# Optimization experiments

Hardware: AMD Instinct MI355X
Metric: run time of the kernel (lower is better)

Reference implementation:

```python
import jax, jax.numpy as jnp
import numpy as np
import math

N, C, T, V = 8, 256, 128, 25
H, HC = 8, 32            # num_heads, head_channels
W, DIL = 3, 1            # window, dilation
O = 256                  # out_channels
PAD = (W + (W - 1) * (DIL - 1) - 1) // 2
B, L = N * T, W * V


def _ln(x, g, b):
    m = jnp.mean(x, -1, keepdims=True)
    v = jnp.var(x, -1, keepdims=True)
    return (x - m) * jax.lax.rsqrt(v + 1e-5) * g + b


def setup_inputs() -> dict:
    key = jax.random.key(0)
    ks = iter(jax.random.split(key, 40))
    def w(shape):
        return jax.random.normal(next(ks), shape, jnp.float32) * 0.02
    d = {"x": jax.random.normal(next(ks), (N, C, T, V), jnp.float32)}
    d.update(
        ln1_g=jnp.ones((C,)), ln1_b=jnp.zeros((C,)),
        Wq=w((C, C)), bq=jnp.zeros((C,)), Wqa=w((C, H)), bqa=jnp.zeros((H,)),
        Wk=w((C, C)), bk=jnp.zeros((C,)), Wka=w((C, H)), bka=jnp.zeros((H,)),
        Wv=w((C, C)), bv=jnp.zeros((C,)), Wt=w((C, C)), bt=jnp.zeros((C,)),
        Wp=w((C, C)), bp=jnp.zeros((C,)),
        ffn_g=jnp.ones((C,)), ffn_b=jnp.zeros((C,)),
        W1=w((C, C)), b1=jnp.zeros((C,)), W2=w((C, C)), b2=jnp.zeros((C,)),
        tn_g=jnp.ones((C,)), tn_b=jnp.zeros((C,)),
        c1_w=w((C, O)), c1_b=jnp.zeros((O,)),
        c2_w=w((W, O, O)), c2_b=jnp.zeros((O,)),
    )
    return d


def reference(x, ln1_g, ln1_b, Wq, bq, Wqa, bqa, Wk, bk, Wka, bka, Wv, bv,
              Wt, bt, Wp, bp, ffn_g, ffn_b, W1, b1, W2, b2, tn_g, tn_b,
              c1_w, c1_b, c2_w, c2_b):
    scale = 1.0 / math.sqrt(HC)
    # ---- Unfold over time: build window of frames around each t (nn.Unfold) ----
    xp = jnp.pad(x, ((0, 0), (0, 0), (PAD, PAD), (0, 0)))
    win = jnp.stack([jax.lax.dynamic_slice_in_dim(xp, k * DIL, T, 2) for k in range(W)], 2)  # (N,C,W,T,V)
    seq = win.transpose(0, 3, 2, 4, 1).reshape(B, L, C)  # (N*T, W*V, C)

    sep = lambda z: z.reshape(B, L, H, HC).transpose(0, 2, 1, 3)  # (B,H,L,HC)
    grp = lambda z: z.transpose(0, 2, 1, 3).reshape(B, -1, C)

    # ---- SpatioTemporalAttention (eval: dropouts off) ----
    nx = _ln(seq, ln1_g, ln1_b)
    q = nx @ Wq + bq                                            # (B,L,C)
    qw = jax.nn.softmax((q @ Wqa + bqa).transpose(0, 2, 1) * scale, axis=-1)  # (B,H,L)
    pq = jnp.einsum('bhl,bhlc->bhc', qw, sep(q)).reshape(B, 1, C)             # pooled query
    keys = nx @ Wk + bk
    kw = jax.nn.softmax(((keys * pq) @ Wka + bka).transpose(0, 2, 1) * scale, axis=-1)
    pk = jnp.einsum('bhl,bhlc->bhc', kw, sep(keys))             # pooled key (B,H,HC)
    vals = sep(nx @ Wv + bv)
    kv = grp(vals * pk[:, :, None, :]) @ Wt + bt                # (B,L,C)
    attn = (kv + q) @ Wp + bp                                   # residual-in-heads == plain add

    # ---- AttentionBranch residual + FFN ----
    att = attn + seq
    f = _ln(att, ffn_g, ffn_b)
    y = jax.nn.gelu(f @ W1 + b1, approximate=False) @ W2 + b2 + att  # (B,L,C)

    # ---- temporal branch: LN -> regroup frames -> 1x1 conv -> GELU -> (W,1) conv stride W ----
    t5 = _ln(y, tn_g, tn_b).reshape(N, T, W, V, C)
    h = jax.nn.gelu(t5 @ c1_w + c1_b, approximate=False)        # (N,T,W,V,O)
    out = jnp.einsum('ntwvi,wio->ntvo', h, c2_w) + c2_b         # stride==kernel conv == window contraction
    return out.transpose(0, 3, 1, 2)                            # (N,O,T,V)
```

## Files before the change

kernel.cpp:

```cpp
#include <hip/hip_runtime.h>


#define DI __device__ __forceinline__

constexpr int CC   = 256;
constexpr int CL   = 75;
constexpr int CV   = 25;
constexpr int CT   = 128;
constexpr int TP   = 130;
constexpr int MPAD = 8 * TP * CV;
constexpr int MBL  = 1024 * CL;
constexpr int MOUT = 8 * CT * CV;
constexpr float SM_SCALE = 0.17677669529663687f;

typedef __bf16 bf16x8 __attribute__((ext_vector_type(8)));
typedef float f32x4 __attribute__((ext_vector_type(4)));

DI float bf2f(unsigned short u) { return __uint_as_float(((unsigned)u) << 16); }
DI float bf2f_lo(unsigned u) { return __uint_as_float(u << 16); }
DI float bf2f_hi(unsigned u) { return __uint_as_float(u & 0xffff0000u); }
DI unsigned short f2bf(float f) {
  unsigned u = __float_as_uint(f);
  u += 0x7fffu + ((u >> 16) & 1u);
  return (unsigned short)(u >> 16);
}
DI unsigned packbf(float a, float b) {
  return (unsigned)f2bf(a) | ((unsigned)f2bf(b) << 16);
}
DI float geluf(float x) { return 0.5f * x * (1.f + erff(x * 0.70710678118654752440f)); }

DI void gll16(const unsigned short* g, unsigned short* l) {
  __builtin_amdgcn_global_load_lds(
      (const __attribute__((address_space(1))) unsigned int*)g,
      (__attribute__((address_space(3))) unsigned int*)l, 16, 0, 0);
}

DI int arow(int r) {
  int b = r / CL;
  int l = r - b * CL;
  int w = l / CV;
  int v = l - w * CV;
  int t = b & (CT - 1);
  int n = b >> 7;
  return (n * TP + t + w) * CV + v;
}

__global__ __launch_bounds__(256) void k_transpose(const float* __restrict__ x,
                                                   unsigned short* __restrict__ xtp) {
  __shared__ float tile[32][33];
  const int n = blockIdx.z;
  const int c0 = blockIdx.x * 32;
  const int tv0 = blockIdx.y * 32;
  const int tx = threadIdx.x & 31, ty = threadIdx.x >> 5;
#pragma unroll
  for (int j = 0; j < 32; j += 8) {
    tile[ty + j][tx] = x[((size_t)(n * CC + c0 + ty + j)) * 3200 + tv0 + tx];
  }
  __syncthreads();
#pragma unroll
  for (int j = 0; j < 32; j += 8) {
    int tv = tv0 + ty + j;
    int st = tv / CV, v = tv - st * CV;
    size_t row = ((size_t)n * TP + st + 1) * CV + v;
    xtp[row * CC + c0 + tx] = f2bf(tile[tx][ty + j]);
  }
}

__global__ __launch_bounds__(256) void k_zero_pad(unsigned short* __restrict__ xtp) {
  int i = blockIdx.x * 256 + threadIdx.x;
  int c = i & 255;
  int rid = i >> 8;
  int n = rid / 50;
  int rem = rid - n * 50;
  int side = rem / 25;
  int v = rem - side * 25;
  size_t row = ((size_t)n * TP + side * (TP - 1)) * CV + v;
  xtp[row * CC + c] = 0;
}

struct TJobs {
  const float* src[10];
  unsigned short* dst[10];
// ... 20 lines not shown
__global__ __launch_bounds__(256) void k_wtwp(const float* __restrict__ Wt,
                                              const float* __restrict__ Wp,
                                              unsigned short* __restrict__ fused) {
  __shared__ float wrow[256];
  const int k = blockIdx.x, n = threadIdx.x;
  wrow[n] = Wt[(size_t)k * 256 + n];
  __syncthreads();
  float acc = 0.f;
  for (int j = 0; j < 256; ++j) acc = fmaf(wrow[j], Wp[(size_t)j * 256 + n], acc);
  fused[(size_t)n * 512 + k] = f2bf(acc);
}

__global__ __launch_bounds__(256) void k_bias2(const float* __restrict__ bt,
                                               const float* __restrict__ Wp,
                                               const float* __restrict__ bp,
                                               const float* __restrict__ bq,
                                               const float* __restrict__ bk,
                                               const float* __restrict__ bv,
                                               float* __restrict__ bias2,
                                               float* __restrict__ bias3) {
  const int n = threadIdx.x;
  float acc = bp[n];
  for (int j = 0; j < 256; ++j) acc = fmaf(bt[j], Wp[(size_t)j * 256 + n], acc);
  bias2[n] = acc;
  bias3[n] = bq[n];
  bias3[256 + n] = bk[n];
  bias3[512 + n] = bv[n];
}

__global__ __launch_bounds__(256) void k_ln4(const unsigned short* __restrict__ X,
                                             const float* __restrict__ g,
                                             const float* __restrict__ b,
                                             unsigned short* __restrict__ Y) {
  const int row = blockIdx.x * 4 + (threadIdx.x >> 6);
  const int lane = threadIdx.x & 63;
  const uint2 u = *(const uint2*)(X + (size_t)row * CC + lane * 4);
  const float x0 = bf2f_lo(u.x), x1 = bf2f_hi(u.x), x2 = bf2f_lo(u.y), x3 = bf2f_hi(u.y);
  float s = x0 + x1 + x2 + x3;
  float q = x0 * x0 + x1 * x1 + x2 * x2 + x3 * x3;
#pragma unroll
  for (int o = 32; o; o >>= 1) { s += __shfl_xor(s, o); q += __shfl_xor(q, o); }
  const float mean = s * (1.f / CC);
  const float var = q * (1.f / CC) - mean * mean;
  const float rs = rsqrtf(var + 1e-5f);
  const float4 g4 = *(const float4*)(g + lane * 4);
  const float4 b4 = *(const float4*)(b + lane * 4);
  uint2 o2;
  o2.x = packbf((x0 - mean) * rs * g4.x + b4.x, (x1 - mean) * rs * g4.y + b4.y);
  o2.y = packbf((x2 - mean) * rs * g4.z + b4.z, (x3 - mean) * rs * g4.w + b4.w);
  *(uint2*)(Y + (size_t)row * CC + lane * 4) = o2;
}

template <int AMODE, int EPI, int KD, bool MULTI>
__global__ __launch_bounds__(512) void k_mgemm(const unsigned short* __restrict__ A,
                                               const unsigned short* __restrict__ BwT,
                                               const float* __restrict__ bias,
                                               unsigned short* __restrict__ Cout,
                                               float* __restrict__ FOut,
                                               int M) {
  if constexpr (MULTI) {
    const int z = blockIdx.y;
    BwT += (size_t)z * (256 * 256);
    bias += z * 256;
    Cout += (size_t)z * MPAD * CC;
  }
  __shared__ unsigned short SH[20480];
  const int tid = threadIdx.x;
  const int lane = tid & 63;
  const int wid = tid >> 6;
  const int wm = wid >> 2, wn = wid & 3;
  const int r0 = blockIdx.x * 64;
  f32x4 acc[2][4] = {};

  const bool sa = tid < 256;
  const int rA = r0 + (tid >> 2);
  const int seg8 = (tid & 3) * 8;
  const bool valid = sa && (rA < M);
  int hrb = 0;
  if (valid && AMODE == 4) {
    const int nb = rA / 3200, rr = rA - nb * 3200;
    const int tq = rr / 25, vq = rr - tq * 25;
    hrb = (nb * CT + tq) * CL + vq;
  }

  auto loadA4 = [&](int k0) -> uint4 {
    uint4 u = make_uint4(0, 0, 0, 0);
    if (!valid) return u;
    const int w = k0 >> 8;
    u = *(const uint4*)(A + (size_t)(hrb + w * CV) * CC + (k0 & 255) + seg8);
    return u;
  };
  auto stageB = [&](int buf, int k0) {
    unsigned short* bs = SH + 4096 + buf * 8192;
#pragma unroll
    for (int pp = 0; pp < 2; ++pp) {
      const int s = tid + pp * 512;
      gll16(BwT + (size_t)(s >> 2) * KD + k0 + (s & 3) * 8, bs + s * 8);
    }
  };
  auto stageAg = [&](int buf, int k0) {
    if (valid) gll16(A + (size_t)rA * CC + k0 + seg8, SH + buf * 2048 + tid * 8);
  };

  stageB(0, 0);
  if constexpr (AMODE == 0) {
    stageAg(0, 0);
  } else {
    const uint4 a0 = loadA4(0);
    if (sa) *(uint4*)(SH + tid * 8) = a0;
  }
  __syncthreads();

  constexpr int NT = KD / 32;
  int cur = 0;
  for (int t = 0; t < NT; ++t) {
    const int nxt = cur ^ 1;
    const bool more = (t + 1 < NT);
    uint4 an;
    if (more) {
      stageB(nxt, (t + 1) * 32);
      if constexpr (AMODE == 0) stageAg(nxt, (t + 1) * 32);
      else an = loadA4((t + 1) * 32);
    }
    const unsigned short* as = SH + cur * 2048;
    const unsigned short* bs = SH + 4096 + cur * 8192;
    bf16x8 af[2], bfr[4];
#pragma unroll
    for (int mi = 0; mi < 2; ++mi)
      af[mi] = *(const bf16x8*)(as + (wm * 32 + mi * 16 + (lane & 15)) * 32 + (lane >> 4) * 8);
#pragma unroll
    for (int ni = 0; ni < 4; ++ni)
      bfr[ni] = *(const bf16x8*)(bs + (wn * 64 + ni * 16 + (lane & 15)) * 32 + (lane >> 4) * 8);
#pragma unroll
    for (int mi = 0; mi < 2; ++mi)
#pragma unroll
      for (int ni = 0; ni < 4; ++ni)
        acc[mi][ni] = __builtin_amdgcn_mfma_f32_16x16x32_bf16(af[mi], bfr[ni], acc[mi][ni], 0, 0, 0);
    if (more) {
      if constexpr (AMODE != 0) {
        if (sa) *(uint4*)(SH + nxt * 2048 + tid * 8) = an;
      }
      __syncthreads();
      cur = nxt;
    }
  }

  const int ln15 = lane & 15, lq = lane >> 4;
  if constexpr (EPI == 4) {
#pragma unroll
    for (int mi = 0; mi < 2; ++mi) {
#pragma unroll
      for (int ni = 0; ni < 4; ++ni) {
        const int col = wn * 64 + ni * 16 + ln15;
        const float bcol = bias[col];
        const int rbase = r0 + wm * 32 + mi * 16 + lq * 4;
        const int nb = rbase / 3200, rr = rbase - nb * 3200;
        float4 v;
        v.x = acc[mi][ni][0] + bcol;
        v.y = acc[mi][ni][1] + bcol;
        v.z = acc[mi][ni][2] + bcol;
        v.w = acc[mi][ni][3] + bcol;
        *(float4*)(FOut + (size_t)nb * 819200 + (size_t)col * 3200 + rr) = v;
      }
    }
  } else {
    constexpr int LDC = 260;
    __syncthreads();
#pragma unroll
    for (int mi = 0; mi < 2; ++mi) {
#pragma unroll
      for (int ni = 0; ni < 4; ++ni) {
        const int col = wn * 64 + ni * 16 + ln15;
        const float bcol = bias[col];
#pragma unroll
        for (int rg = 0; rg < 4; ++rg) {
          const int lrow = wm * 32 + mi * 16 + lq * 4 + rg;
          SH[lrow * LDC + col] = f2bf(acc[mi][ni][rg] + bcol);
        }
      }
    }
    __syncthreads();
#pragma unroll
    for (int i = 0; i < 4; ++i) {
      const int idx = tid + i * 512;
      const int row = idx >> 5, ch = idx & 31;
      const int gr = r0 + row;
      if (gr < M)
        *(uint4*)(Cout + (size_t)gr * CC + ch * 8) = *(const uint4*)&SH[row * LDC + ch * 8];
    }
  }
}

__global__ __launch_bounds__(512) void k_chain(
    const unsigned short* __restrict__ VP, const unsigned short* __restrict__ QP,
    const float* __restrict__ PK, const unsigned short* __restrict__ XTP,
    const unsigned short* __restrict__ fusedB, const float* __restrict__ bias2,
    const unsigned short* __restrict__ W1T, const float* __restrict__ b1,
    const unsigned short* __restrict__ W2T, const float* __restrict__ b2,
    const float* __restrict__ ffn_g, const float* __restrict__ ffn_b,
    const unsigned short* __restrict__ c1wT, const float* __restrict__ c1b,
    const float* __restrict__ tn_g, const float* __restrict__ tn_b,
    unsigned short* __restrict__ Hout) {
  constexpr int LDC = 264;
  __shared__ unsigned short SH[16896 + 4096 + 16384];
  unsigned short* ACT = SH;
  unsigned short* AS = SH + 16896;
  unsigned short* BS = SH + 16896 + 4096;
  const int tid = threadIdx.x;
  const int lane = tid & 63, wid = tid >> 6;
  const int wm = wid >> 2, wn = wid & 3;
  const int ln15 = lane & 15, lq = lane >> 4;
  const int r0 = blockIdx.x * 64;

  const bool sa = tid < 256;
  const int rA = r0 + (tid >> 2);
  const int seg8 = (tid & 3) * 8;
  int ar = 0, bb = 0;
  if (sa) { ar = arow(rA); bb = rA / CL; }

  auto stageB = [&](const unsigned short* BwT, int KD, int buf, int k0) {
    unsigned short* bs = BS + buf * 8192;
#pragma unroll
    for (int pp = 0; pp < 2; ++pp) {
      const int s = tid + pp * 512;
      gll16(BwT + (size_t)(s >> 2) * KD + k0 + (s & 3) * 8, bs + s * 8);
    }
  };
  auto loadA5 = [&](int k0) -> uint4 {
    uint4 u = make_uint4(0, 0, 0, 0);
    if (!sa) return u;
    if (k0 < 256) {
      const int kg = k0 + seg8;
      const uint4 t4 = *(const uint4*)(VP + (size_t)ar * CC + kg);
      const float* sv = PK + bb * CC + kg;
      const float4 s0 = *(const float4*)sv;
      const float4 s1 = *(const float4*)(sv + 4);
      u.x = packbf(bf2f_lo(t4.x) * s0.x, bf2f_hi(t4.x) * s0.y);
      u.y = packbf(bf2f_lo(t4.y) * s0.z, bf2f_hi(t4.y) * s0.w);
      u.z = packbf(bf2f_lo(t4.z) * s1.x, bf2f_hi(t4.z) * s1.y);
      u.w = packbf(bf2f_lo(t4.w) * s1.z, bf2f_hi(t4.w) * s1.w);
    } else {
      u = *(const uint4*)(QP + (size_t)ar * CC + (k0 - 256) + seg8);
    }
    return u;
  };
  auto ln_inplace = [&](const float* g, const float* b) {
    const float4 g4 = *(const float4*)(g + lane * 4);
    const float4 b4 = *(const float4*)(b + lane * 4);
#pragma unroll
    for (int rr = 0; rr < 8; ++rr) {
      const int row = wid * 8 + rr;
      const uint2 u = *(const uint2*)(ACT + row * LDC + lane * 4);
      const float x0 = bf2f_lo(u.x), x1 = bf2f_hi(u.x);
      const float x2 = bf2f_lo(u.y), x3 = bf2f_hi(u.y);
      float s = x0 + x1 + x2 + x3;
      float q = x0 * x0 + x1 * x1 + x2 * x2 + x3 * x3;
#pragma unroll
      for (int o = 32; o; o >>= 1) { s += __shfl_xor(s, o); q += __shfl_xor(q, o); }
      const float mean = s * (1.f / CC);
      const float var = q * (1.f / CC) - mean * mean;
      const float rs = rsqrtf(var + 1e-5f);
      uint2 o2;
      o2.x = packbf((x0 - mean) * rs * g4.x + b4.x, (x1 - mean) * rs * g4.y + b4.y);
      o2.y = packbf((x2 - mean) * rs * g4.z + b4.z, (x3 - mean) * rs * g4.w + b4.w);
      *(uint2*)(ACT + row * LDC + lane * 4) = o2;
    }
  };
  auto gemmACT = [&](const unsigned short* BwT, f32x4 (&a)[2][4]) {
    int c2 = 0;
    for (int t = 0; t < 8; ++t) {
      if (t + 1 < 8) stageB(BwT, 256, c2 ^ 1, (t + 1) * 32);
      bf16x8 af[2], bfr[4];
#pragma unroll
      for (int mi = 0; mi < 2; ++mi)
        af[mi] = *(const bf16x8*)(ACT + (wm * 32 + mi * 16 + ln15) * LDC + t * 32 + lq * 8);
#pragma unroll
      for (int ni = 0; ni < 4; ++ni)
        bfr[ni] = *(const bf16x8*)(BS + c2 * 8192 + (wn * 64 + ni * 16 + ln15) * 32 + lq * 8);
#pragma unroll
      for (int mi = 0; mi < 2; ++mi)
#pragma unroll
        for (int ni = 0; ni < 4; ++ni)
          a[mi][ni] = __builtin_amdgcn_mfma_f32_16x16x32_bf16(af[mi], bfr[ni], a[mi][ni], 0, 0, 0);
      if (t + 1 < 8) { __syncthreads(); c2 ^= 1; }
    }
  };

  f32x4 acc[2][4] = {};
  stageB(fusedB, 512, 0, 0);
  { uint4 a0 = loadA5(0); if (sa) *(uint4*)(AS + tid * 8) = a0; }
  __syncthreads();
  int cur = 0;
  for (int t = 0; t < 16; ++t) {
    const int nxt = cur ^ 1;
    const bool more = (t + 1 < 16);
    uint4 an;
    if (more) { stageB(fusedB, 512, nxt, (t + 1) * 32); an = loadA5((t + 1) * 32); }
    bf16x8 af[2], bfr[4];
#pragma unroll
    for (int mi = 0; mi < 2; ++mi)
      af[mi] = *(const bf16x8*)(AS + cur * 2048 + (wm * 32 + mi * 16 + ln15) * 32 + lq * 8);
#pragma unroll
    for (int ni = 0; ni < 4; ++ni)
      bfr[ni] = *(const bf16x8*)(BS + cur * 8192 + (wn * 64 + ni * 16 + ln15) * 32 + lq * 8);
#pragma unroll
    for (int mi = 0; mi < 2; ++mi)
#pragma unroll
      for (int ni = 0; ni < 4; ++ni)
        acc[mi][ni] = __builtin_amdgcn_mfma_f32_16x16x32_bf16(af[mi], bfr[ni], acc[mi][ni], 0, 0, 0);
    if (more) {
      if (sa) *(uint4*)(AS + nxt * 2048 + tid * 8) = an;
      __syncthreads();
      cur = nxt;
    }
  }
  f32x4 attres[2][4];
#pragma unroll
  for (int mi = 0; mi < 2; ++mi) {
#pragma unroll
    for (int ni = 0; ni < 4; ++ni) {
      const int col = wn * 64 + ni * 16 + ln15;
      const float bcol = bias2[col];
#pragma unroll
      for (int rg = 0; rg < 4; ++rg) {
        const int r = r0 + wm * 32 + mi * 16 + lq * 4 + rg;
        attres[mi][ni][rg] = acc[mi][ni][rg] + bcol + bf2f(XTP[(size_t)arow(r) * CC + col]);
      }
    }
  }
  stageB(W1T, 256, 0, 0);
#pragma unroll
  for (int mi = 0; mi < 2; ++mi)
#pragma unroll
    for (int ni = 0; ni < 4; ++ni) {
      const int col = wn * 64 + ni * 16 + ln15;
#pragma unroll
      for (int rg = 0; rg < 4; ++rg)
        ACT[(wm * 32 + mi * 16 + lq * 4 + rg) * LDC + col] = f2bf(attres[mi][ni][rg]);
    }
  __syncthreads();
  ln_inplace(ffn_g, ffn_b);
  __syncthreads();

  f32x4 acc2[2][4] = {};
  gemmACT(W1T, acc2);
  stageB(W2T, 256, 0, 0);
  __syncthreads();
#pragma unroll
  for (int mi = 0; mi < 2; ++mi)
#pragma unroll
    for (int ni = 0; ni < 4; ++ni) {
      const int col = wn * 64 + ni * 16 + ln15;
      const float bcol = b1[col];
#pragma unroll
      for (int rg = 0; rg < 4; ++rg)
        ACT[(wm * 32 + mi * 16 + lq * 4 + rg) * LDC + col] = f2bf(geluf(acc2[mi][ni][rg] + bcol));
    }
  __syncthreads();

  f32x4 acc3[2][4] = {};
  gemmACT(W2T, acc3);
  stageB(c1wT, 256, 0, 0);
  __syncthreads();
#pragma unroll
  for (int mi = 0; mi < 2; ++mi)
#pragma unroll
    for (int ni = 0; ni < 4; ++ni) {
      const int col = wn * 64 + ni * 16 + ln15;
      const float bcol = b2[col];
#pragma unroll
      for (int rg = 0; rg < 4; ++rg)
        ACT[(wm * 32 + mi * 16 + lq * 4 + rg) * LDC + col] =
            f2bf(acc3[mi][ni][rg] + bcol + attres[mi][ni][rg]);
    }
  __syncthreads();
  ln_inplace(tn_g, tn_b);
  __syncthreads();

  f32x4 acc4[2][4] = {};
  gemmACT(c1wT, acc4);
  __syncthreads();
#pragma unroll
  for (int mi = 0; mi < 2; ++mi)
#pragma unroll
    for (int ni = 0; ni < 4; ++ni) {
      const int col = wn * 64 + ni * 16 + ln15;
      const float bcol = c1b[col];
#pragma unroll
      for (int rg = 0; rg < 4; ++rg)
        ACT[(wm * 32 + mi * 16 + lq * 4 + rg) * LDC + col] = f2bf(geluf(acc4[mi][ni][rg] + bcol));
    }
  __syncthreads();
#pragma unroll
  for (int i = 0; i < 4; ++i) {
    const int idx = tid + i * 512;
    const int row = idx >> 5, ch = idx & 31;
    *(uint4*)(Hout + (size_t)(r0 + row) * CC + ch * 8) = *(const uint4*)&ACT[row * LDC + ch * 8];
  }
}

__global__ __launch_bounds__(256) void k_proj8(const unsigned short* __restrict__ SRC,
                                               const float* __restrict__ Wsm,
                                               const float* __restrict__ bsm,
                                               float* __restrict__ OUT) {
  const int r = blockIdx.x * 4 + (threadIdx.x >> 6);
  const int lane = threadIdx.x & 63;
  const int c = lane * 4;
  const uint2 u = *(const uint2*)(SRC + (size_t)r * CC + c);
  const float m0 = bf2f_lo(u.x), m1 = bf2f_hi(u.x), m2 = bf2f_lo(u.y), m3 = bf2f_hi(u.y);
  float p[8] = {};
#pragma unroll
  for (int j = 0; j < 4; ++j) {
    const float mj = (j == 0) ? m0 : (j == 1) ? m1 : (j == 2) ? m2 : m3;
#pragma unroll
    for (int h = 0; h < 8; ++h) p[h] += mj * Wsm[(c + j) * 8 + h];
  }
#pragma unroll
  for (int h = 0; h < 8; ++h) {
#pragma unroll
    for (int o = 32; o; o >>= 1) p[h] += __shfl_down(p[h], o);
  }
  if (lane == 0) {
#pragma unroll
    for (int h = 0; h < 8; ++h) OUT[(size_t)r * 8 + h] = p[h] + bsm[h];
  }
}

template <int SIDE>
__global__ __launch_bounds__(256) void k_attpool(const unsigned short* __restrict__ ROWS,
                                                 const float* __restrict__ QA,
                                                 const float* __restrict__ PQ,
                                                 const float* __restrict__ Wka,
                                                 const float* __restrict__ bka,
                                                 float* __restrict__ OUT) {
  __shared__ unsigned short rows[CL * CC];
  __shared__ float uu[(SIDE == 1) ? 8 * 258 : 8];
  __shared__ float lg[8 * 76];
  __shared__ float inv8[8];
  __shared__ int arl[CL];
  const int b = blockIdx.x;
  const int t = threadIdx.x;

  if (t < CL) arl[t] = arow(b * CL + t);
  __syncthreads();

  for (int i = t; i < CL * 32; i += 256) {
    const int r = i >> 5, seg = i & 31;
    gll16(ROWS + (size_t)arl[r] * CC + seg * 8, &rows[i * 8]);
  }
  if constexpr (SIDE == 0) {
    for (int i = t; i < CL * 2; i += 256) {
      const int l = i >> 1, q = i & 1;
      const float4 v = *(const float4*)(QA + (size_t)arl[l] * 8 + q * 4);
      lg[(q * 4 + 0) * 76 + l] = v.x * SM_SCALE;
      lg[(q * 4 + 1) * 76 + l] = v.y * SM_SCALE;
      lg[(q * 4 + 2) * 76 + l] = v.z * SM_SCALE;
      lg[(q * 4 + 3) * 76 + l] = v.w * SM_SCALE;
    }
  } else {
    for (int i = t; i < CC * 8; i += 256) {
      const int c = i >> 3, h = i & 7;
      uu[h * 258 + c] = PQ[(size_t)b * CC + c] * Wka[c * 8 + h];
    }
  }
  __syncthreads();

  if constexpr (SIDE == 1) {
    const int c0 = (t & 127) * 2;
    for (int i = t; i < CL * 8; i += 256) {
      const int h = i / CL, l = i - h * CL;
      float acc = bka[h];
#pragma unroll 4
      for (int jj = 0; jj < CC; jj += 2) {
        const int c = (c0 + jj) & 255;
        const unsigned pr = *(const unsigned*)&rows[l * CC + c];
        acc = fmaf(bf2f_lo(pr), uu[h * 258 + c], acc);
        acc = fmaf(bf2f_hi(pr), uu[h * 258 + c + 1], acc);
      }
      lg[h * 76 + l] = acc * SM_SCALE;
    }
    __syncthreads();
  }

  if (t < 8) {
    float m = -1e30f;
    for (int l = 0; l < CL; ++l) m = fmaxf(m, lg[t * 76 + l]);
    float s = 0.f;
    for (int l = 0; l < CL; ++l) {
      const float e = __expf(lg[t * 76 + l] - m);
      lg[t * 76 + l] = e;
      s += e;
    }
    inv8[t] = 1.f / s;
  }
  __syncthreads();

  {
    const int h = t >> 5;
    float acc = 0.f;
    for (int l = 0; l < CL; ++l) acc = fmaf(lg[h * 76 + l], bf2f(rows[l * CC + t]), acc);
    OUT[(size_t)b * CC + t] = acc * inv8[h];
  }
}

extern "C" void kernel_launch(void* const* d_in, const int* in_sizes, int n_in,
                              void* d_out, int out_size, void* d_ws, size_t ws_size,
                              hipStream_t stream) {
  const float* x = (const float*)d_in[0];
  const float* ln1_g = (const float*)d_in[1];
  const float* ln1_b = (const float*)d_in[2];
  const float* Wq = (const float*)d_in[3];
  const float* bq = (const float*)d_in[4];
  const float* Wqa = (const float*)d_in[5];
  const float* bqa = (const float*)d_in[6];
  const float* Wk = (const float*)d_in[7];
  const float* bk = (const float*)d_in[8];
  const float* Wka = (const float*)d_in[9];
  const float* bka = (const float*)d_in[10];
  const float* Wv = (const float*)d_in[11];
  const float* bv = (const float*)d_in[12];
  const float* Wt = (const float*)d_in[13];
  const float* bt = (const float*)d_in[14];
  const float* Wp = (const float*)d_in[15];
  const float* bp = (const float*)d_in[16];
  const float* ffn_g = (const float*)d_in[17];
  const float* ffn_b = (const float*)d_in[18];
  const float* W1 = (const float*)d_in[19];
  const float* b1 = (const float*)d_in[20];
  const float* W2 = (const float*)d_in[21];
  const float* b2 = (const float*)d_in[22];
  const float* tn_g = (const float*)d_in[23];
  const float* tn_b = (const float*)d_in[24];
  const float* c1w = (const float*)d_in[25];
  const float* c1b = (const float*)d_in[26];
  const float* c2w = (const float*)d_in[27];
  const float* c2b = (const float*)d_in[28];
  float* out = (float*)d_out;

  char* wp = (char*)d_ws;
  auto alloc = [&](size_t bytes) -> char* {
    char* p = wp;
    wp += (bytes + 255) & ~(size_t)255;
    return p;
  };
  unsigned short* XTP = (unsigned short*)alloc((size_t)MPAD * CC * 2);
  unsigned short* LNXP = (unsigned short*)alloc((size_t)MPAD * CC * 2);
  unsigned short* QKVP = (unsigned short*)alloc((size_t)3 * MPAD * CC * 2);
  unsigned short* QP = QKVP;
  unsigned short* KP = QKVP + (size_t)MPAD * CC;
  unsigned short* VP = QKVP + (size_t)2 * MPAD * CC;
  unsigned short* Hb = (unsigned short*)alloc((size_t)MBL * CC * 2);
  float* QA = (float*)alloc((size_t)MPAD * 8 * 4);
  float* PQ = (float*)alloc((size_t)1024 * CC * 4);
  float* PK = (float*)alloc((size_t)1024 * CC * 4);
  unsigned short* WqkvT = (unsigned short*)alloc((size_t)3 * 256 * 256 * 2);
  unsigned short* W1T = (unsigned short*)alloc(256 * 256 * 2);
  unsigned short* W2T = (unsigned short*)alloc(256 * 256 * 2);
  unsigned short* c1wT = (unsigned short*)alloc(256 * 256 * 2);
  unsigned short* c2wT = (unsigned short*)alloc(256 * 768 * 2);
  unsigned short* fusedB = (unsigned short*)alloc(256 * 512 * 2);
  float* bias2 = (float*)alloc(256 * 4);
  float* bias3 = (float*)alloc(768 * 4);

  TJobs J;
  const float* srcs[10] = {Wq, Wk, Wv, W1, W2, c1w, c2w, c2w + 65536, c2w + 131072, Wp};
  unsigned short* dsts[10] = {WqkvT, WqkvT + 65536, WqkvT + 131072, W1T, W2T, c1wT,
                              c2wT, c2wT, c2wT, fusedB};
  const int strides[10] = {256, 256, 256, 256, 256, 256, 768, 768, 768, 512};
  const int offs[10] = {0, 0, 0, 0, 0, 0, 0, 256, 512, 256};
  for (int i = 0; i < 10; ++i) {
    J.src[i] = srcs[i]; J.dst[i] = dsts[i]; J.stride[i] = strides[i]; J.off[i] = offs[i];
  }
  k_wtrans<<<dim3(8, 8, 10), 256, 0, stream>>>(J);
  k_wtwp<<<256, 256, 0, stream>>>(Wt, Wp, fusedB);
  k_bias2<<<1, 256, 0, stream>>>(bt, Wp, bp, bq, bk, bv, bias2, bias3);

  k_transpose<<<dim3(8, 100, 8), 256, 0, stream>>>(x, XTP);
  k_zero_pad<<<400, 256, 0, stream>>>(XTP);
  k_ln4<<<MPAD / 4, 256, 0, stream>>>(XTP, ln1_g, ln1_b, LNXP);

  const int gP = (MPAD + 63) / 64;
  const int gO = MOUT / 64;
  k_mgemm<0, 0, 256, true><<<dim3(gP, 3), 512, 0, stream>>>(
      LNXP, WqkvT, bias3, QKVP, nullptr, MPAD);

  k_proj8<<<MPAD / 4, 256, 0, stream>>>(QP, Wqa, bqa, QA);
  k_attpool<0><<<1024, 256, 0, stream>>>(QP, QA, nullptr, nullptr, nullptr, PQ);
  k_attpool<1><<<1024, 256, 0, stream>>>(KP, nullptr, PQ, Wka, bka, PK);

  k_chain<<<MBL / 64, 512, 0, stream>>>(VP, QP, PK, XTP, fusedB, bias2,
                                        W1T, b1, W2T, b2, ffn_g, ffn_b,
                                        c1wT, c1b, tn_g, tn_b, Hb);

  k_mgemm<4, 4, 768, false><<<gO, 512, 0, stream>>>(Hb, c2wT, c2b, nullptr, out, MOUT);
}
```

Before: 311.8 us.

## Load GEMM operands directly from global into registers, dropping LDS staging

Both the generic GEMM kernel and the fused chain kernel stop staging A and B tiles through shared memory with async global-to-LDS copies and barriers. Each wave now loads its MFMA fragments straight from global memory into registers, double-buffered in software. Shared memory shrinks to the output tile, the attention residual is kept packed as bf16 to save registers, and launch bounds request 4 blocks per CU to raise occupancy. In exchange, B tiles are reloaded redundantly by each wave, reads are less coalesced, and the residual loses precision by going through bf16.

```diff
diff --git a/kernel.cpp b/kernel.cpp
--- a/kernel.cpp
+++ b/kernel.cpp
@@ -28,6 +28,7 @@
   return (unsigned)f2bf(a) | ((unsigned)f2bf(b) << 16);
 }
 DI float geluf(float x) { return 0.5f * x * (1.f + erff(x * 0.70710678118654752440f)); }
+DI bf16x8 u4bf(uint4 u) { bf16x8 r; __builtin_memcpy(&r, &u, 16); return r; }
 
 DI void gll16(const unsigned short* g, unsigned short* l) {
   __builtin_amdgcn_global_load_lds(
@@ -154,100 +155,79 @@
 }
 
 template <int AMODE, int EPI, int KD, bool MULTI>
-__global__ __launch_bounds__(512) void k_mgemm(const unsigned short* __restrict__ A,
-                                               const unsigned short* __restrict__ BwT,
-                                               const float* __restrict__ bias,
-                                               unsigned short* __restrict__ Cout,
-                                               float* __restrict__ FOut,
-                                               int M) {
+__global__ __launch_bounds__(512, 4) void k_mgemm(const unsigned short* __restrict__ A,
+                                                  const unsigned short* __restrict__ BwT,
+                                                  const float* __restrict__ bias,
+                                                  unsigned short* __restrict__ Cout,
+                                                  float* __restrict__ FOut,
+                                                  int M) {
   if constexpr (MULTI) {
     const int z = blockIdx.y;
     BwT += (size_t)z * (256 * 256);
     bias += z * 256;
     Cout += (size_t)z * MPAD * CC;
   }
-  __shared__ unsigned short SH[20480];
+  constexpr int LDC = 264;
+  __shared__ unsigned short CTile[(EPI == 0) ? 64 * LDC : 64];
   const int tid = threadIdx.x;
-  const int lane = tid & 63;
-  const int wid = tid >> 6;
+  const int lane = tid & 63, wid = tid >> 6;
   const int wm = wid >> 2, wn = wid & 3;
+  const int ln15 = lane & 15, lq = lane >> 4;
   const int r0 = blockIdx.x * 64;
+
+  int rowm[2];
+#pragma unroll
+  for (int mi = 0; mi < 2; ++mi) {
+    int r = r0 + wm * 32 + mi * 16 + ln15;
+    if (r >= M) r = M - 1;
+    if constexpr (AMODE == 0) {
+      rowm[mi] = r;
+    } else {
+      const int nb = r / 3200, rr = r - nb * 3200;
+      const int tq = rr / 25, vq = rr - tq * 25;
+      rowm[mi] = (nb * CT + tq) * CL + vq;
+    }
+  }
+
+  auto loadA2 = [&](int t, bf16x8* dst) {
+#pragma unroll
+    for (int mi = 0; mi < 2; ++mi) {
+      if constexpr (AMODE == 0) {
+        dst[mi] = u4bf(*(const uint4*)(A + (size_t)rowm[mi] * CC + t * 32 + lq * 8));
+      } else {
+        const int w = t >> 3, kk = (t & 7) * 32;
+        dst[mi] = u4bf(*(const uint4*)(A + (size_t)(rowm[mi] + w * CV) * CC + kk + lq * 8));
+      }
+    }
+  };
+  auto loadB4 = [&](int t, bf16x8* dst) {
+#pragma unroll
+    for (int ni = 0; ni < 4; ++ni)
+      dst[ni] = u4bf(*(const uint4*)(BwT + (size_t)(wn * 64 + ni * 16 + ln15) * KD + t * 32 + lq * 8));
+  };
+
   f32x4 acc[2][4] = {};
-
-  const bool sa = tid < 256;
-  const int rA = r0 + (tid >> 2);
-  const int seg8 = (tid & 3) * 8;
-  const bool valid = sa && (rA < M);
-  int hrb = 0;
-  if (valid && AMODE == 4) {
-    const int nb = rA / 3200, rr = rA - nb * 3200;
-    const int tq = rr / 25, vq = rr - tq * 25;
-    hrb = (nb * CT + tq) * CL + vq;
-  }
-
-  auto loadA4 = [&](int k0) -> uint4 {
-    uint4 u = make_uint4(0, 0, 0, 0);
-    if (!valid) return u;
-    const int w = k0 >> 8;
-    u = *(const uint4*)(A + (size_t)(hrb + w * CV) * CC + (k0 & 255) + seg8);
-    return u;
-  };
-  auto stageB = [&](int buf, int k0) {
-    unsigned short* bs = SH + 4096 + buf * 8192;
-#pragma unroll
-    for (int pp = 0; pp < 2; ++pp) {
-      const int s = tid + pp * 512;
-      gll16(BwT + (size_t)(s >> 2) * KD + k0 + (s & 3) * 8, bs + s * 8);
-    }
-  };
-  auto stageAg = [&](int buf, int k0) {
-    if (valid) gll16(A + (size_t)rA * CC + k0 + seg8, SH + buf * 2048 + tid * 8);
-  };
-
-  stageB(0, 0);
-  if constexpr (AMODE == 0) {
-    stageAg(0, 0);
-  } else {
-    const uint4 a0 = loadA4(0);
-    if (sa) *(uint4*)(SH + tid * 8) = a0;
-  }
-  __syncthreads();
-
+  bf16x8 aA[2], aB[2], bA[4], bB[4];
+  loadA2(0, aA);
+  loadB4(0, bA);
   constexpr int NT = KD / 32;
-  int cur = 0;
-  for (int t = 0; t < NT; ++t) {
-    const int nxt = cur ^ 1;
-    const bool more = (t + 1 < NT);
-    uint4 an;
-    if (more) {
-      stageB(nxt, (t + 1) * 32);
-      if constexpr (AMODE == 0) stageAg(nxt, (t + 1) * 32);
-      else an = loadA4((t + 1) * 32);
-    }
-    const unsigned short* as = SH + cur * 2048;
-    const unsigned short* bs = SH + 4096 + cur * 8192;
-    bf16x8 af[2], bfr[4];
+#pragma unroll
+  for (int t = 0; t < NT; t += 2) {
+    loadA2(t + 1, aB);
+    loadB4(t + 1, bB);
 #pragma unroll
     for (int mi = 0; mi < 2; ++mi)
-      af[mi] = *(const bf16x8*)(as + (wm * 32 + mi * 16 + (lane & 15)) * 32 + (lane >> 4) * 8);
-#pragma unroll
-    for (int ni = 0; ni < 4; ++ni)
-      bfr[ni] = *(const bf16x8*)(bs + (wn * 64 + ni * 16 + (lane & 15)) * 32 + (lane >> 4) * 8);
+#pragma unroll
+      for (int ni = 0; ni < 4; ++ni)
+        acc[mi][ni] = __builtin_amdgcn_mfma_f32_16x16x32_bf16(aA[mi], bA[ni], acc[mi][ni], 0, 0, 0);
+    if (t + 2 < NT) { loadA2(t + 2, aA); loadB4(t + 2, bA); }
 #pragma unroll
     for (int mi = 0; mi < 2; ++mi)
 #pragma unroll
       for (int ni = 0; ni < 4; ++ni)
-        acc[mi][ni] = __builtin_amdgcn_mfma_f32_16x16x32_bf16(af[mi], bfr[ni], acc[mi][ni], 0, 0, 0);
-    if (more) {
-      if constexpr (AMODE != 0) {
-        if (sa) *(uint4*)(SH + nxt * 2048 + tid * 8) = an;
-      }
-      __syncthreads();
-      cur = nxt;
-    }
-  }
-
-  const int ln15 = lane & 15, lq = lane >> 4;
+        acc[mi][ni] = __builtin_amdgcn_mfma_f32_16x16x32_bf16(aB[mi], bB[ni], acc[mi][ni], 0, 0, 0);
+  }
+
   if constexpr (EPI == 4) {
 #pragma unroll
     for (int mi = 0; mi < 2; ++mi) {
@@ -266,8 +246,6 @@
       }
     }
   } else {
-    constexpr int LDC = 260;
-    __syncthreads();
 #pragma unroll
     for (int mi = 0; mi < 2; ++mi) {
 #pragma unroll
@@ -277,7 +255,7 @@
 #pragma unroll
         for (int rg = 0; rg < 4; ++rg) {
           const int lrow = wm * 32 + mi * 16 + lq * 4 + rg;
-          SH[lrow * LDC + col] = f2bf(acc[mi][ni][rg] + bcol);
+          CTile[lrow * LDC + col] = f2bf(acc[mi][ni][rg] + bcol);
         }
       }
     }
@@ -288,12 +266,12 @@
       const int row = idx >> 5, ch = idx & 31;
       const int gr = r0 + row;
       if (gr < M)
-        *(uint4*)(Cout + (size_t)gr * CC + ch * 8) = *(const uint4*)&SH[row * LDC + ch * 8];
-    }
-  }
-}
-
-__global__ __launch_bounds__(512) void k_chain(
+        *(uint4*)(Cout + (size_t)gr * CC + ch * 8) = *(const uint4*)&CTile[row * LDC + ch * 8];
+    }
+  }
+}
+
+__global__ __launch_bounds__(512, 4) void k_chain(
     const unsigned short* __restrict__ VP, const unsigned short* __restrict__ QP,
     const float* __restrict__ PK, const unsigned short* __restrict__ XTP,
     const unsigned short* __restrict__ fusedB, const float* __restrict__ bias2,
@@ -304,47 +282,45 @@
     const float* __restrict__ tn_g, const float* __restrict__ tn_b,
     unsigned short* __restrict__ Hout) {
   constexpr int LDC = 264;
-  __shared__ unsigned short SH[16896 + 4096 + 16384];
-  unsigned short* ACT = SH;
-  unsigned short* AS = SH + 16896;
-  unsigned short* BS = SH + 16896 + 4096;
+  __shared__ unsigned short ACT[64 * LDC];
   const int tid = threadIdx.x;
   const int lane = tid & 63, wid = tid >> 6;
   const int wm = wid >> 2, wn = wid & 3;
   const int ln15 = lane & 15, lq = lane >> 4;
   const int r0 = blockIdx.x * 64;
 
-  const bool sa = tid < 256;
-  const int rA = r0 + (tid >> 2);
-  const int seg8 = (tid & 3) * 8;
-  int ar = 0, bb = 0;
-  if (sa) { ar = arow(rA); bb = rA / CL; }
-
-  auto stageB = [&](const unsigned short* BwT, int KD, int buf, int k0) {
-    unsigned short* bs = BS + buf * 8192;
-#pragma unroll
-    for (int pp = 0; pp < 2; ++pp) {
-      const int s = tid + pp * 512;
-      gll16(BwT + (size_t)(s >> 2) * KD + k0 + (s & 3) * 8, bs + s * 8);
-    }
+  int arm[2], bbm[2];
+#pragma unroll
+  for (int mi = 0; mi < 2; ++mi) {
+    const int r = r0 + wm * 32 + mi * 16 + ln15;
+    arm[mi] = arow(r);
+    bbm[mi] = r / CL;
+  }
+
+  auto loadB4 = [&](const unsigned short* BwT, int KD, int t, bf16x8* dst) {
+#pragma unroll
+    for (int ni = 0; ni < 4; ++ni)
+      dst[ni] = u4bf(*(const uint4*)(BwT + (size_t)(wn * 64 + ni * 16 + ln15) * KD + t * 32 + lq * 8));
   };
-  auto loadA5 = [&](int k0) -> uint4 {
-    uint4 u = make_uint4(0, 0, 0, 0);
-    if (!sa) return u;
-    if (k0 < 256) {
-      const int kg = k0 + seg8;
-      const uint4 t4 = *(const uint4*)(VP + (size_t)ar * CC + kg);
-      const float* sv = PK + bb * CC + kg;
-      const float4 s0 = *(const float4*)sv;
-      const float4 s1 = *(const float4*)(sv + 4);
-      u.x = packbf(bf2f_lo(t4.x) * s0.x, bf2f_hi(t4.x) * s0.y);
-      u.y = packbf(bf2f_lo(t4.y) * s0.z, bf2f_hi(t4.y) * s0.w);
-      u.z = packbf(bf2f_lo(t4.z) * s1.x, bf2f_hi(t4.z) * s1.y);
-      u.w = packbf(bf2f_lo(t4.w) * s1.z, bf2f_hi(t4.w) * s1.w);
-    } else {
-      u = *(const uint4*)(QP + (size_t)ar * CC + (k0 - 256) + seg8);
-    }
-    return u;
+  auto loadA1 = [&](int t, bf16x8* dst) {
+#pragma unroll
+    for (int mi = 0; mi < 2; ++mi) {
+      if (t < 8) {
+        const int kg = t * 32 + lq * 8;
+        const uint4 u = *(const uint4*)(VP + (size_t)arm[mi] * CC + kg);
+        const float* sv = PK + bbm[mi] * CC + kg;
+        const float4 s0 = *(const float4*)sv;
+        const float4 s1 = *(const float4*)(sv + 4);
+        uint4 o;
+        o.x = packbf(bf2f_lo(u.x) * s0.x, bf2f_hi(u.x) * s0.y);
+        o.y = packbf(bf2f_lo(u.y) * s0.z, bf2f_hi(u.y) * s0.w);
+        o.z = packbf(bf2f_lo(u.z) * s1.x, bf2f_hi(u.z) * s1.y);
+        o.w = packbf(bf2f_lo(u.w) * s1.z, bf2f_hi(u.w) * s1.w);
+        dst[mi] = u4bf(o);
+      } else {
+        dst[mi] = u4bf(*(const uint4*)(QP + (size_t)arm[mi] * CC + (t - 8) * 32 + lq * 8));
+      }
+    }
   };
   auto ln_inplace = [&](const float* g, const float* b) {
     const float4 g4 = *(const float4*)(g + lane * 4);
@@ -369,84 +345,80 @@
     }
   };
   auto gemmACT = [&](const unsigned short* BwT, f32x4 (&a)[2][4]) {
-    int c2 = 0;
-    for (int t = 0; t < 8; ++t) {
-      if (t + 1 < 8) stageB(BwT, 256, c2 ^ 1, (t + 1) * 32);
-      bf16x8 af[2], bfr[4];
+    bf16x8 bA[4], bB[4];
+    loadB4(BwT, 256, 0, bA);
+#pragma unroll
+    for (int t = 0; t < 8; t += 2) {
+      loadB4(BwT, 256, t + 1, bB);
+      bf16x8 afA[2];
 #pragma unroll
       for (int mi = 0; mi < 2; ++mi)
-        af[mi] = *(const bf16x8*)(ACT + (wm * 32 + mi * 16 + ln15) * LDC + t * 32 + lq * 8);
-#pragma unroll
-      for (int ni = 0; ni < 4; ++ni)
-        bfr[ni] = *(const bf16x8*)(BS + c2 * 8192 + (wn * 64 + ni * 16 + ln15) * 32 + lq * 8);
+        afA[mi] = *(const bf16x8*)(ACT + (wm * 32 + mi * 16 + ln15) * LDC + t * 32 + lq * 8);
 #pragma unroll
       for (int mi = 0; mi < 2; ++mi)
 #pragma unroll
         for (int ni = 0; ni < 4; ++ni)
-          a[mi][ni] = __builtin_amdgcn_mfma_f32_16x16x32_bf16(af[mi], bfr[ni], a[mi][ni], 0, 0, 0);
-      if (t + 1 < 8) { __syncthreads(); c2 ^= 1; }
+          a[mi][ni] = __builtin_amdgcn_mfma_f32_16x16x32_bf16(afA[mi], bA[ni], a[mi][ni], 0, 0, 0);
+      if (t + 2 < 8) loadB4(BwT, 256, t + 2, bA);
+      bf16x8 afB[2];
+#pragma unroll
+      for (int mi = 0; mi < 2; ++mi)
+        afB[mi] = *(const bf16x8*)(ACT + (wm * 32 + mi * 16 + ln15) * LDC + (t + 1) * 32 + lq * 8);
+#pragma unroll
+      for (int mi = 0; mi < 2; ++mi)
+#pragma unroll
+        for (int ni = 0; ni < 4; ++ni)
+          a[mi][ni] = __builtin_amdgcn_mfma_f32_16x16x32_bf16(afB[mi], bB[ni], a[mi][ni], 0, 0, 0);
     }
   };
 
   f32x4 acc[2][4] = {};
-  stageB(fusedB, 512, 0, 0);
-  { uint4 a0 = loadA5(0); if (sa) *(uint4*)(AS + tid * 8) = a0; }
-  __syncthreads();
-  int cur = 0;
-  for (int t = 0; t < 16; ++t) {
-    const int nxt = cur ^ 1;
-    const bool more = (t + 1 < 16);
-    uint4 an;
-    if (more) { stageB(fusedB, 512, nxt, (t + 1) * 32); an = loadA5((t + 1) * 32); }
-    bf16x8 af[2], bfr[4];
-#pragma unroll
-    for (int mi = 0; mi < 2; ++mi)
-      af[mi] = *(const bf16x8*)(AS + cur * 2048 + (wm * 32 + mi * 16 + ln15) * 32 + lq * 8);
-#pragma unroll
-    for (int ni = 0; ni < 4; ++ni)
-      bfr[ni] = *(const bf16x8*)(BS + cur * 8192 + (wn * 64 + ni * 16 + ln15) * 32 + lq * 8);
-#pragma unroll
-    for (int mi = 0; mi < 2; ++mi)
-#pragma unroll
-      for (int ni = 0; ni < 4; ++ni)
-        acc[mi][ni] = __builtin_amdgcn_mfma_f32_16x16x32_bf16(af[mi], bfr[ni], acc[mi][ni], 0, 0, 0);
-    if (more) {
-      if (sa) *(uint4*)(AS + nxt * 2048 + tid * 8) = an;
-      __syncthreads();
-      cur = nxt;
-    }
-  }
-  f32x4 attres[2][4];
+  {
+    bf16x8 aA[2], aB[2], bA[4], bB[4];
+    loadA1(0, aA);
+    loadB4(fusedB, 512, 0, bA);
+#pragma unroll
+    for (int t = 0; t < 16; t += 2) {
+      loadA1(t + 1, aB);
+      loadB4(fusedB, 512, t + 1, bB);
+#pragma unroll
+      for (int mi = 0; mi < 2; ++mi)
+#pragma unroll
+        for (int ni = 0; ni < 4; ++ni)
+          acc[mi][ni] = __builtin_amdgcn_mfma_f32_16x16x32_bf16(aA[mi], bA[ni], acc[mi][ni], 0, 0, 0);
+      if (t + 2 < 16) { loadA1(t + 2, aA); loadB4(fusedB, 512, t + 2, bA); }
+#pragma unroll
+      for (int mi = 0; mi < 2; ++mi)
+#pragma unroll
+        for (int ni = 0; ni < 4; ++ni)
+          acc[mi][ni] = __builtin_amdgcn_mfma_f32_16x16x32_bf16(aB[mi], bB[ni], acc[mi][ni], 0, 0, 0);
+    }
+  }
+  uint2 attp[2][4];
 #pragma unroll
   for (int mi = 0; mi < 2; ++mi) {
 #pragma unroll
     for (int ni = 0; ni < 4; ++ni) {
       const int col = wn * 64 + ni * 16 + ln15;
       const float bcol = bias2[col];
+      float v[4];
 #pragma unroll
       for (int rg = 0; rg < 4; ++rg) {
         const int r = r0 + wm * 32 + mi * 16 + lq * 4 + rg;
-        attres[mi][ni][rg] = acc[mi][ni][rg] + bcol + bf2f(XTP[(size_t)arow(r) * CC + col]);
+        v[rg] = acc[mi][ni][rg] + bcol + bf2f(XTP[(size_t)arow(r) * CC + col]);
       }
-    }
-  }
-  stageB(W1T, 256, 0, 0);
-#pragma unroll
-  for (int mi = 0; mi < 2; ++mi)
-#pragma unroll
-    for (int ni = 0; ni < 4; ++ni) {
-      const int col = wn * 64 + ni * 16 + ln15;
+      attp[mi][ni] = make_uint2(packbf(v[0], v[1]), packbf(v[2], v[3]));
 #pragma unroll
       for (int rg = 0; rg < 4; ++rg)
-        ACT[(wm * 32 + mi * 16 + lq * 4 + rg) * LDC + col] = f2bf(attres[mi][ni][rg]);
-    }
+        ACT[(wm * 32 + mi * 16 + lq * 4 + rg) * LDC + col] = f2bf(v[rg]);
+    }
+  }
   __syncthreads();
   ln_inplace(ffn_g, ffn_b);
   __syncthreads();
 
   f32x4 acc2[2][4] = {};
   gemmACT(W1T, acc2);
-  stageB(W2T, 256, 0, 0);
   __syncthreads();
 #pragma unroll
   for (int mi = 0; mi < 2; ++mi)
@@ -462,7 +434,6 @@
 
   f32x4 acc3[2][4] = {};
   gemmACT(W2T, acc3);
-  stageB(c1wT, 256, 0, 0);
   __syncthreads();
 #pragma unroll
   for (int mi = 0; mi < 2; ++mi)
@@ -470,10 +441,13 @@
     for (int ni = 0; ni < 4; ++ni) {
       const int col = wn * 64 + ni * 16 + ln15;
       const float bcol = b2[col];
-#pragma unroll
-      for (int rg = 0; rg < 4; ++rg)
-        ACT[(wm * 32 + mi * 16 + lq * 4 + rg) * LDC + col] =
-            f2bf(acc3[mi][ni][rg] + bcol + attres[mi][ni][rg]);
+      const float a0 = bf2f_lo(attp[mi][ni].x), a1 = bf2f_hi(attp[mi][ni].x);
+      const float a2 = bf2f_lo(attp[mi][ni].y), a3 = bf2f_hi(attp[mi][ni].y);
+      const int lrow = wm * 32 + mi * 16 + lq * 4;
+      ACT[(lrow + 0) * LDC + col] = f2bf(acc3[mi][ni][0] + bcol + a0);
+      ACT[(lrow + 1) * LDC + col] = f2bf(acc3[mi][ni][1] + bcol + a1);
+      ACT[(lrow + 2) * LDC + col] = f2bf(acc3[mi][ni][2] + bcol + a2);
+      ACT[(lrow + 3) * LDC + col] = f2bf(acc3[mi][ni][3] + bcol + a3);
     }
   __syncthreads();
   ln_inplace(tn_g, tn_b);
```

Result: slower. 510.8 us (+63.8%).

## Load chain A-operand straight to registers and fuse query logit projection into attpool

Applied to the files above, without the earlier changes.

The first GEMM in k_chain now loads and scales the V/Q operand directly into MFMA registers per lane, instead of staging it through a shared-memory buffer. This frees LDS, and launch bounds now request higher occupancy. The separate k_proj8 kernel is removed and its per-head query logits are computed inside k_attpool<0>, which recomputes them from rows already staged in LDS and saves a launch plus the QA round trip. The epilogue also precomputes the residual row indices and writes ACT in the same loop. The trade-offs are redundant global loads across the wn warps and extra logit work in attpool.

```diff
diff --git a/kernel.cpp b/kernel.cpp
--- a/kernel.cpp
+++ b/kernel.cpp
@@ -28,6 +28,7 @@
   return (unsigned)f2bf(a) | ((unsigned)f2bf(b) << 16);
 }
 DI float geluf(float x) { return 0.5f * x * (1.f + erff(x * 0.70710678118654752440f)); }
+DI bf16x8 u4bf(uint4 u) { bf16x8 r; __builtin_memcpy(&r, &u, 16); return r; }
 
 DI void gll16(const unsigned short* g, unsigned short* l) {
   __builtin_amdgcn_global_load_lds(
@@ -293,7 +294,7 @@
   }
 }
 
-__global__ __launch_bounds__(512) void k_chain(
+__global__ __launch_bounds__(512, 4) void k_chain(
     const unsigned short* __restrict__ VP, const unsigned short* __restrict__ QP,
     const float* __restrict__ PK, const unsigned short* __restrict__ XTP,
     const unsigned short* __restrict__ fusedB, const float* __restrict__ bias2,
@@ -304,21 +305,26 @@
     const float* __restrict__ tn_g, const float* __restrict__ tn_b,
     unsigned short* __restrict__ Hout) {
   constexpr int LDC = 264;
-  __shared__ unsigned short SH[16896 + 4096 + 16384];
+  __shared__ unsigned short SH[16896 + 16384];
   unsigned short* ACT = SH;
-  unsigned short* AS = SH + 16896;
-  unsigned short* BS = SH + 16896 + 4096;
+  unsigned short* BS = SH + 16896;
   const int tid = threadIdx.x;
   const int lane = tid & 63, wid = tid >> 6;
   const int wm = wid >> 2, wn = wid & 3;
   const int ln15 = lane & 15, lq = lane >> 4;
   const int r0 = blockIdx.x * 64;
 
-  const bool sa = tid < 256;
-  const int rA = r0 + (tid >> 2);
-  const int seg8 = (tid & 3) * 8;
-  int ar = 0, bb = 0;
-  if (sa) { ar = arow(rA); bb = rA / CL; }
+  int arm[2], bbm[2];
+#pragma unroll
+  for (int mi = 0; mi < 2; ++mi) {
+    const int r = r0 + wm * 32 + mi * 16 + ln15;
+    arm[mi] = arow(r);
+    bbm[mi] = r / CL;
+  }
+  int xrow[8];
+#pragma unroll
+  for (int i = 0; i < 8; ++i)
+    xrow[i] = arow(r0 + wm * 32 + (i >> 2) * 16 + lq * 4 + (i & 3));
 
   auto stageB = [&](const unsigned short* BwT, int KD, int buf, int k0) {
     unsigned short* bs = BS + buf * 8192;
@@ -328,23 +334,36 @@
       gll16(BwT + (size_t)(s >> 2) * KD + k0 + (s & 3) * 8, bs + s * 8);
     }
   };
-  auto loadA5 = [&](int k0) -> uint4 {
-    uint4 u = make_uint4(0, 0, 0, 0);
-    if (!sa) return u;
-    if (k0 < 256) {
-      const int kg = k0 + seg8;
-      const uint4 t4 = *(const uint4*)(VP + (size_t)ar * CC + kg);
-      const float* sv = PK + bb * CC + kg;
-      const float4 s0 = *(const float4*)sv;
-      const float4 s1 = *(const float4*)(sv + 4);
-      u.x = packbf(bf2f_lo(t4.x) * s0.x, bf2f_hi(t4.x) * s0.y);
-      u.y = packbf(bf2f_lo(t4.y) * s0.z, bf2f_hi(t4.y) * s0.w);
-      u.z = packbf(bf2f_lo(t4.z) * s1.x, bf2f_hi(t4.z) * s1.y);
-      u.w = packbf(bf2f_lo(t4.w) * s1.z, bf2f_hi(t4.w) * s1.w);
-    } else {
-      u = *(const uint4*)(QP + (size_t)ar * CC + (k0 - 256) + seg8);
-    }
-    return u;
+  auto loadA1 = [&](int t, bf16x8* dst) {
+#pragma unroll
+    for (int mi = 0; mi < 2; ++mi) {
+      if (t < 8) {
+        const int kg = t * 32 + lq * 8;
+        const uint4 u = *(const uint4*)(VP + (size_t)arm[mi] * CC + kg);
+        const float* sv = PK + bbm[mi] * CC + kg;
+        const float4 s0 = *(const float4*)sv;
+        const float4 s1 = *(const float4*)(sv + 4);
+        uint4 o;
+        o.x = packbf(bf2f_lo(u.x) * s0.x, bf2f_hi(u.x) * s0.y);
+        o.y = packbf(bf2f_lo(u.y) * s0.z, bf2f_hi(u.y) * s0.w);
+        o.z = packbf(bf2f_lo(u.z) * s1.x, bf2f_hi(u.z) * s1.y);
+        o.w = packbf(bf2f_lo(u.w) * s1.z, bf2f_hi(u.w) * s1.w);
+        dst[mi] = u4bf(o);
+      } else {
+        dst[mi] = u4bf(*(const uint4*)(QP + (size_t)arm[mi] * CC + (t - 8) * 32 + lq * 8));
+      }
+    }
+  };
+  auto mfmaB = [&](int buf, bf16x8* af, f32x4 (&a)[2][4]) {
+    bf16x8 bfr[4];
+#pragma unroll
+    for (int ni = 0; ni < 4; ++ni)
+      bfr[ni] = *(const bf16x8*)(BS + buf * 8192 + (wn * 64 + ni * 16 + ln15) * 32 + lq * 8);
+#pragma unroll
+    for (int mi = 0; mi < 2; ++mi)
+#pragma unroll
+      for (int ni = 0; ni < 4; ++ni)
+        a[mi][ni] = __builtin_amdgcn_mfma_f32_16x16x32_bf16(af[mi], bfr[ni], a[mi][ni], 0, 0, 0);
   };
   auto ln_inplace = [&](const float* g, const float* b) {
     const float4 g4 = *(const float4*)(g + lane * 4);
@@ -372,50 +391,34 @@
     int c2 = 0;
     for (int t = 0; t < 8; ++t) {
       if (t + 1 < 8) stageB(BwT, 256, c2 ^ 1, (t + 1) * 32);
-      bf16x8 af[2], bfr[4];
+      bf16x8 af[2];
 #pragma unroll
       for (int mi = 0; mi < 2; ++mi)
         af[mi] = *(const bf16x8*)(ACT + (wm * 32 + mi * 16 + ln15) * LDC + t * 32 + lq * 8);
-#pragma unroll
-      for (int ni = 0; ni < 4; ++ni)
-        bfr[ni] = *(const bf16x8*)(BS + c2 * 8192 + (wn * 64 + ni * 16 + ln15) * 32 + lq * 8);
-#pragma unroll
-      for (int mi = 0; mi < 2; ++mi)
-#pragma unroll
-        for (int ni = 0; ni < 4; ++ni)
-          a[mi][ni] = __builtin_amdgcn_mfma_f32_16x16x32_bf16(af[mi], bfr[ni], a[mi][ni], 0, 0, 0);
+      mfmaB(c2, af, a);
       if (t + 1 < 8) { __syncthreads(); c2 ^= 1; }
     }
   };
 
   f32x4 acc[2][4] = {};
-  stageB(fusedB, 512, 0, 0);
-  { uint4 a0 = loadA5(0); if (sa) *(uint4*)(AS + tid * 8) = a0; }
-  __syncthreads();
-  int cur = 0;
-  for (int t = 0; t < 16; ++t) {
-    const int nxt = cur ^ 1;
-    const bool more = (t + 1 < 16);
-    uint4 an;
-    if (more) { stageB(fusedB, 512, nxt, (t + 1) * 32); an = loadA5((t + 1) * 32); }
-    bf16x8 af[2], bfr[4];
-#pragma unroll
-    for (int mi = 0; mi < 2; ++mi)
-      af[mi] = *(const bf16x8*)(AS + cur * 2048 + (wm * 32 + mi * 16 + ln15) * 32 + lq * 8);
-#pragma unroll
-    for (int ni = 0; ni < 4; ++ni)
-      bfr[ni] = *(const bf16x8*)(BS + cur * 8192 + (wn * 64 + ni * 16 + ln15) * 32 + lq * 8);
-#pragma unroll
-    for (int mi = 0; mi < 2; ++mi)
-#pragma unroll
-      for (int ni = 0; ni < 4; ++ni)
-        acc[mi][ni] = __builtin_amdgcn_mfma_f32_16x16x32_bf16(af[mi], bfr[ni], acc[mi][ni], 0, 0, 0);
-    if (more) {
-      if (sa) *(uint4*)(AS + nxt * 2048 + tid * 8) = an;
-      __syncthreads();
-      cur = nxt;
-    }
-  }
+  {
+    bf16x8 aA[2], aB[2];
+    stageB(fusedB, 512, 0, 0);
+    loadA1(0, aA);
+    __syncthreads();
+#pragma unroll
+    for (int t = 0; t < 16; t += 2) {
+      if (t + 1 < 16) { stageB(fusedB, 512, 1, (t + 1) * 32); loadA1(t + 1, aB); }
+      mfmaB(0, aA, acc);
+      if (t + 1 < 16) __syncthreads();
+      if (t + 2 < 16) { stageB(fusedB, 512, 0, (t + 2) * 32); loadA1(t + 2, aA); }
+      if (t + 1 < 16) {
+        mfmaB(1, aB, acc);
+        if (t + 2 < 16) __syncthreads();
+      }
+    }
+  }
+  stageB(W1T, 256, 0, 0);
   f32x4 attres[2][4];
 #pragma unroll
   for (int mi = 0; mi < 2; ++mi) {
@@ -425,21 +428,12 @@
       const float bcol = bias2[col];
 #pragma unroll
       for (int rg = 0; rg < 4; ++rg) {
-        const int r = r0 + wm * 32 + mi * 16 + lq * 4 + rg;
-        attres[mi][ni][rg] = acc[mi][ni][rg] + bcol + bf2f(XTP[(size_t)arow(r) * CC + col]);
+        attres[mi][ni][rg] =
+            acc[mi][ni][rg] + bcol + bf2f(XTP[(size_t)xrow[mi * 4 + rg] * CC + col]);
+        ACT[(wm * 32 + mi * 16 + lq * 4 + rg) * LDC + col] = f2bf(attres[mi][ni][rg]);
       }
     }
   }
-  stageB(W1T, 256, 0, 0);
-#pragma unroll
-  for (int mi = 0; mi < 2; ++mi)
-#pragma unroll
-    for (int ni = 0; ni < 4; ++ni) {
-      const int col = wn * 64 + ni * 16 + ln15;
-#pragma unroll
-      for (int rg = 0; rg < 4; ++rg)
-        ACT[(wm * 32 + mi * 16 + lq * 4 + rg) * LDC + col] = f2bf(attres[mi][ni][rg]);
-    }
   __syncthreads();
   ln_inplace(ffn_g, ffn_b);
   __syncthreads();
@@ -501,42 +495,14 @@
   }
 }
 
-__global__ __launch_bounds__(256) void k_proj8(const unsigned short* __restrict__ SRC,
-                                               const float* __restrict__ Wsm,
-                                               const float* __restrict__ bsm,
-                                               float* __restrict__ OUT) {
-  const int r = blockIdx.x * 4 + (threadIdx.x >> 6);
-  const int lane = threadIdx.x & 63;
-  const int c = lane * 4;
-  const uint2 u = *(const uint2*)(SRC + (size_t)r * CC + c);
-  const float m0 = bf2f_lo(u.x), m1 = bf2f_hi(u.x), m2 = bf2f_lo(u.y), m3 = bf2f_hi(u.y);
-  float p[8] = {};
-#pragma unroll
-  for (int j = 0; j < 4; ++j) {
-    const float mj = (j == 0) ? m0 : (j == 1) ? m1 : (j == 2) ? m2 : m3;
-#pragma unroll
-    for (int h = 0; h < 8; ++h) p[h] += mj * Wsm[(c + j) * 8 + h];
-  }
-#pragma unroll
-  for (int h = 0; h < 8; ++h) {
-#pragma unroll
-    for (int o = 32; o; o >>= 1) p[h] += __shfl_down(p[h], o);
-  }
-  if (lane == 0) {
-#pragma unroll
-    for (int h = 0; h < 8; ++h) OUT[(size_t)r * 8 + h] = p[h] + bsm[h];
-  }
-}
-
 template <int SIDE>
 __global__ __launch_bounds__(256) void k_attpool(const unsigned short* __restrict__ ROWS,
-                                                 const float* __restrict__ QA,
                                                  const float* __restrict__ PQ,
-                                                 const float* __restrict__ Wka,
-                                                 const float* __restrict__ bka,
+                                                 const float* __restrict__ W8,
+                                                 const float* __restrict__ b8,
                                                  float* __restrict__ OUT) {
   __shared__ unsigned short rows[CL * CC];
-  __shared__ float uu[(SIDE == 1) ? 8 * 258 : 8];
+  __shared__ float uu[8 * 258];
   __shared__ float lg[8 * 76];
   __shared__ float inv8[8];
   __shared__ int arl[CL];
@@ -550,28 +516,20 @@
     const int r = i >> 5, seg = i & 31;
     gll16(ROWS + (size_t)arl[r] * CC + seg * 8, &rows[i * 8]);
   }
-  if constexpr (SIDE == 0) {
-    for (int i = t; i < CL * 2; i += 256) {
-      const int l = i >> 1, q = i & 1;
-      const float4 v = *(const float4*)(QA + (size_t)arl[l] * 8 + q * 4);
-      lg[(q * 4 + 0) * 76 + l] = v.x * SM_SCALE;
-      lg[(q * 4 + 1) * 76 + l] = v.y * SM_SCALE;
-      lg[(q * 4 + 2) * 76 + l] = v.z * SM_SCALE;
-      lg[(q * 4 + 3) * 76 + l] = v.w * SM_SCALE;
-    }
-  } else {
-    for (int i = t; i < CC * 8; i += 256) {
-      const int c = i >> 3, h = i & 7;
-      uu[h * 258 + c] = PQ[(size_t)b * CC + c] * Wka[c * 8 + h];
-    }
-  }
-  __syncthreads();
-
-  if constexpr (SIDE == 1) {
+  for (int i = t; i < CC * 8; i += 256) {
+    const int c = i >> 3, h = i & 7;
+    if constexpr (SIDE == 0)
+      uu[h * 258 + c] = W8[c * 8 + h];
+    else
+      uu[h * 258 + c] = PQ[(size_t)b * CC + c] * W8[c * 8 + h];
+  }
+  __syncthreads();
+
+  {
     const int c0 = (t & 127) * 2;
     for (int i = t; i < CL * 8; i += 256) {
       const int h = i / CL, l = i - h * CL;
-      float acc = bka[h];
+      float acc = b8[h];
 #pragma unroll 4
       for (int jj = 0; jj < CC; jj += 2) {
         const int c = (c0 + jj) & 255;
@@ -581,8 +539,8 @@
       }
       lg[h * 76 + l] = acc * SM_SCALE;
     }
-    __syncthreads();
-  }
+  }
+  __syncthreads();
 
   if (t < 8) {
     float m = -1e30f;
@@ -652,7 +610,6 @@
   unsigned short* KP = QKVP + (size_t)MPAD * CC;
   unsigned short* VP = QKVP + (size_t)2 * MPAD * CC;
   unsigned short* Hb = (unsigned short*)alloc((size_t)MBL * CC * 2);
-  float* QA = (float*)alloc((size_t)MPAD * 8 * 4);
   float* PQ = (float*)alloc((size_t)1024 * CC * 4);
   float* PK = (float*)alloc((size_t)1024 * CC * 4);
   unsigned short* WqkvT = (unsigned short*)alloc((size_t)3 * 256 * 256 * 2);
@@ -686,9 +643,8 @@
   k_mgemm<0, 0, 256, true><<<dim3(gP, 3), 512, 0, stream>>>(
       LNXP, WqkvT, bias3, QKVP, nullptr, MPAD);
 
-  k_proj8<<<MPAD / 4, 256, 0, stream>>>(QP, Wqa, bqa, QA);
-  k_attpool<0><<<1024, 256, 0, stream>>>(QP, QA, nullptr, nullptr, nullptr, PQ);
-  k_attpool<1><<<1024, 256, 0, stream>>>(KP, nullptr, PQ, Wka, bka, PK);
+  k_attpool<0><<<1024, 256, 0, stream>>>(QP, nullptr, Wqa, bqa, PQ);
+  k_attpool<1><<<1024, 256, 0, stream>>>(KP, PQ, Wka, bka, PK);
 
   k_chain<<<MBL / 64, 512, 0, stream>>>(VP, QP, PK, XTP, fusedB, bias2,
                                         W1T, b1, W2T, b2, ffn_g, ffn_b,
```

New measurement: 336.3 us. +7.9%, slower.
